# Kernel tuning notes

Measured on AMD Instinct MI355X. Metric: run time of the kernel, lower is better.

The kernel has to match this reference:

```python
import jax, jax.numpy as jnp
import numpy as np
import math

FS, N_FFT, NUM_BANDS, NUM_BINS = 16000, 512, 31, 257
H = 96  # dim_hidden

def band_partition():
    f_min, f_max = FS / N_FFT, FS / 2.0
    z_min = 69.0 + 12.0 * math.log2(f_min / 440.0)
    z_max = 69.0 + 12.0 * math.log2(f_max / 440.0)
    z = np.linspace(z_min, z_max, NUM_BANDS + 2)
    f_points = 440.0 * 2.0 ** ((z - 69.0) / 12.0)
    bins = np.round(f_points * N_FFT / FS).astype(np.int64)
    bins[0] = 0
    bands = []
    for i in range(NUM_BANDS):
        s = max(0, int(bins[i]))
        e = min(NUM_BINS, int(bins[i + 2]) + 1)
        if e <= s:
            e = s + 1
        bands.append((s, e))
    return bands

BANDS = band_partition()

def hann(L):
    # torch.hann_window default (periodic=True)
    return 0.5 - 0.5 * jnp.cos(2.0 * jnp.pi * jnp.arange(L, dtype=jnp.float32) / L)

def chan_ln(x, eps=1e-5):
    # AdaNorm2d assumed = LayerNorm over channel dim, no affine
    m = jnp.mean(x, axis=1, keepdims=True)
    v = jnp.var(x, axis=1, keepdims=True)
    return (x - m) * jax.lax.rsqrt(v + eps)

def prelu(x, a):
    return jnp.where(x >= 0, x, a * x)

def setup_inputs() -> dict:
    key = jax.random.key(0)
    ks = jax.random.split(key, 20)
    B, T = 4, 1000
    return {
        'mix_repr': jax.random.normal(ks[0], (B, H, NUM_BINS, T), jnp.float32),
        'spin': jax.random.normal(ks[1], (B, 64, NUM_BINS, T), jnp.float32),
        'doa': jax.random.normal(ks[2], (B, 36), jnp.float32),
        'enc_w': jax.random.normal(ks[3], (NUM_BANDS, H, 64), jnp.float32) * 0.05,
        'enc_b': jax.random.normal(ks[4], (NUM_BANDS, H), jnp.float32) * 0.05,
        'enc_a': 0.25 * jnp.ones((NUM_BANDS,), jnp.float32),
        'dqg_w': jax.random.normal(ks[5], (NUM_BANDS, 2 * H, 36), jnp.float32) * 0.05,
        'dqg_b': jax.random.normal(ks[6], (NUM_BANDS, 2 * H), jnp.float32) * 0.05,
        'dec_w': jax.random.normal(ks[7], (NUM_BANDS, H, H), jnp.float32) * 0.05,
        'dec_b': jax.random.normal(ks[8], (NUM_BANDS, H), jnp.float32) * 0.05,
        'dec_a': 0.25 * jnp.ones((NUM_BANDS,), jnp.float32),
        'qw': jax.random.normal(ks[9], (H, H), jnp.float32) * 0.05,
        'qb': jax.random.normal(ks[10], (H,), jnp.float32) * 0.05,
        'kw': jax.random.normal(ks[11], (H, H), jnp.float32) * 0.05,
        'kb': jax.random.normal(ks[12], (H,), jnp.float32) * 0.05,
        'vw': jax.random.normal(ks[13], (H, H), jnp.float32) * 0.05,
        'vb': jax.random.normal(ks[14], (H,), jnp.float32) * 0.05,
        'ow': jax.random.normal(ks[15], (H, H), jnp.float32) * 0.05,
        'ob': jax.random.normal(ks[16], (H,), jnp.float32) * 0.05,
    }

def reference(mix_repr, spin, doa, enc_w, enc_b, enc_a, dqg_w, dqg_b,
              dec_w, dec_b, dec_a, qw, qb, kw, kb, vw, vb, ow, ob):
    B, D, F, T = mix_repr.shape
    merged = jnp.zeros((B, H, F, T), mix_repr.dtype)
    wsum = jnp.zeros((F,), mix_repr.dtype)
    for k, (s, e) in enumerate(BANDS):  # fixed set of 31 static ragged bands
        L = e - s
        win = hann(L)
        sub = spin[:, :, s:e, :]                                   # [B,64,L,T]
        feat = jnp.einsum('oc,bcft->boft', enc_w[k], sub) + enc_b[k][None, :, None, None]
        feat = prelu(chan_ln(feat), enc_a[k])
        qp = doa @ dqg_w[k].T + dqg_b[k]                           # [B,2H]
        gamma, beta = qp[:, :H], qp[:, H:]
        tgt = (1.0 + gamma)[:, :, None, None] * feat + beta[:, :, None, None]
        dec = jnp.einsum('oc,bcft->boft', dec_w[k], tgt) + dec_b[k][None, :, None, None]
        dec = prelu(chan_ln(dec), dec_a[k])
        merged = merged.at[:, :, s:e, :].add(dec * win[None, None, :, None])
        wsum = wsum.at[s:e].add(win)
    merged = merged / jnp.clip(wsum, 1e-8)[None, None, :, None]
    # MixtureQueryFusion: 1x1 conv cross-attention gate
    Q = jnp.einsum('oc,bcft->boft', qw, mix_repr) + qb[None, :, None, None]
    K = jnp.einsum('oc,bcft->boft', kw, merged) + kb[None, :, None, None]
    V = jnp.einsum('oc,bcft->boft', vw, merged) + vb[None, :, None, None]
    attn = jax.nn.sigmoid(jnp.sum(Q * K, axis=1, keepdims=True) / jnp.sqrt(jnp.float32(H)))
    attended = V * attn
    out = mix_repr + jnp.einsum('oc,bcft->boft', ow, attended) + ob[None, :, None, None]
    return out
```

## Files before the change

### kernel.cpp

```cpp
#include <hip/hip_runtime.h>
#include <math.h>

#define NBANDS 31
#define FT 257000

typedef __attribute__((ext_vector_type(8))) short bh8;
typedef __attribute__((ext_vector_type(4))) float f4;

__constant__ int d_bs[NBANDS] = {0,1,1,2,2,2,3,3,4,5,6,7,8,10,11,13,16,19,23,27,32,38,45,54,64,76,91,108,128,152,181};
__constant__ int d_be[NBANDS] = {2,3,3,3,4,4,5,6,7,8,9,11,12,14,17,20,24,28,33,39,46,55,65,77,92,109,129,153,182,216,257};

__device__ __forceinline__ unsigned short b16u(float v) {
  __bf16 h = (__bf16)v;
  return __builtin_bit_cast(unsigned short, h);
}
__device__ __forceinline__ unsigned pk2(float a, float b) {
  return (unsigned)b16u(a) | ((unsigned)b16u(b) << 16);
}
__device__ __forceinline__ float hann1(int i, int L) {
  return 0.5f - 0.5f * cosf(6.283185307179586f * (float)i / (float)L);
}

__global__ __launch_bounds__(256) void prep_w(
    const float* __restrict__ enc_w, const float* __restrict__ dec_w,
    const float* __restrict__ qw, const float* __restrict__ kw,
    const float* __restrict__ vw, const float* __restrict__ ow,
    unsigned short* __restrict__ w16) {
  const int stride = gridDim.x * blockDim.x;
  for (int i = blockIdx.x * blockDim.x + threadIdx.x; i < 513024; i += stride) {
    float v;
    if (i < 190464) {
      const int k = i / 6144, r = i - k * 6144;
      const int tile = r >> 9, li = r & 511;
      const int lane = li >> 3, j = li & 7;
      const int g = lane >> 4, n = lane & 15;
      const int mt = tile >> 1, kt = tile & 1;
      v = enc_w[k * 6144 + (mt * 16 + n) * 64 + kt * 32 + g * 8 + j];
    } else if (i < 476160) {
      const int i2 = i - 190464;
      const int k = i2 / 9216, r = i2 - k * 9216;
      const int tile = r >> 9, li = r & 511;
      const int lane = li >> 3, j = li & 7;
      const int g = lane >> 4, n = lane & 15;
      const int mt = tile / 3, kt = tile - mt * 3;
      v = dec_w[k * 9216 + (mt * 16 + n) * 96 + kt * 32 + g * 8 + j];
    } else {
      const int i2 = i - 476160;
      const int a = i2 / 9216, r = i2 - a * 9216;
      const int tile = r >> 9, li = r & 511;
      const int lane = li >> 3, j = li & 7;
      const int g = lane >> 4, n = lane & 15;
      const int mt = tile / 3, kt = tile - mt * 3;
      const float* src = (a == 0) ? qw : (a == 1) ? kw : (a == 2) ? vw : ow;
      v = src[(mt * 16 + n) * 96 + kt * 32 + g * 8 + j];
    }
    w16[i] = b16u(v);
  }
}

__global__ __launch_bounds__(192) void qp_kernel(const float* __restrict__ doa,
                                                 const float* __restrict__ dqg_w,
                                                 const float* __restrict__ dqg_b,
                                                 float* __restrict__ gbuf) {
  const int k = blockIdx.x, b = blockIdx.y;
  const int tid = threadIdx.x;
  __shared__ float sdoa[36];
  if (tid < 36) sdoa[tid] = doa[b * 36 + tid];
  __syncthreads();
  const float* wr = dqg_w + (k * 192 + tid) * 36;
  float acc = dqg_b[k * 192 + tid];
  #pragma unroll
  for (int i = 0; i < 36; ++i) acc = fmaf(wr[i], sdoa[i], acc);
  if (tid < 96) acc += 1.0f;
  gbuf[(k * 4 + b) * 192 + tid] = acc;
}

__global__ __launch_bounds__(320) void tab_kernel(float* __restrict__ ftab) {
  const int f = blockIdx.x * blockDim.x + threadIdx.x;
  if (f >= 257) return;
  int k0 = 0; while (d_be[k0] <= f) ++k0;
  int k1 = k0; while (k1 < NBANDS && d_bs[k1] <= f) ++k1;
  float wsum = 0.f, wn[5];
  for (int k = k0; k < k1; ++k) {
    const float wv = hann1(f - d_bs[k], d_be[k] - d_bs[k]);
    wn[k - k0] = wv; wsum += wv;
  }
  float* o = ftab + f * 8;
  o[0] = (float)k0; o[1] = (float)(k1 - k0); o[2] = 1.0f / fmaxf(wsum, 1e-8f);
  #pragma unroll
  for (int j = 0; j < 5; ++j) o[3 + j] = (j < k1 - k0) ? wn[j] : 0.f;
}

#define LDSWAIT asm volatile("s_waitcnt lgkmcnt(0)" ::: "memory")

__device__ __forceinline__ void init6(f4* acc, const float* s, int off) {
  #pragma unroll
  for (int mt = 0; mt < 6; ++mt) {
    const float4 bb = *reinterpret_cast<const float4*>(s + mt * 16 + off);
    acc[mt] = (f4){bb.x, bb.y, bb.z, bb.w};
  }
}
__device__ __forceinline__ void ln96(const f4* acc, float& mean, float& rs) {
  float s0 = 0.f, s1 = 0.f, s2 = 0.f, s3 = 0.f;
  float q0 = 0.f, q1 = 0.f, q2 = 0.f, q3 = 0.f;
  #pragma unroll
  for (int mt = 0; mt < 6; ++mt) {
    const float a0 = acc[mt][0], a1 = acc[mt][1], a2 = acc[mt][2], a3 = acc[mt][3];
    s0 += a0; s1 += a1; s2 += a2; s3 += a3;
    q0 = fmaf(a0, a0, q0); q1 = fmaf(a1, a1, q1);
    q2 = fmaf(a2, a2, q2); q3 = fmaf(a3, a3, q3);
  }
  float sm = (s0 + s1) + (s2 + s3);
  float sq = (q0 + q1) + (q2 + q3);
  sm += __shfl_xor(sm, 16); sm += __shfl_xor(sm, 32);
  sq += __shfl_xor(sq, 16); sq += __shfl_xor(sq, 32);
  mean = sm * (1.f / 96.f);
  rs = rsqrtf(sq * (1.f / 96.f) - mean * mean + 1e-5f);
}
__device__ __forceinline__ void load6s(bh8* dst, const unsigned short* p, int step9) {
  #pragma unroll
  for (int mt = 0; mt < 6; ++mt)
    dst[mt] = *reinterpret_cast<const bh8*>(p + ((mt * step9) << 9));
}

__global__ __launch_bounds__(256, 3) void fused_mfma(
    const float* __restrict__ mix, const float* __restrict__ spin,
    const unsigned short* __restrict__ enc16, const float* __restrict__ enc_b, const float* __restrict__ enc_a,
    const unsigned short* __restrict__ dec16, const float* __restrict__ dec_b, const float* __restrict__ dec_a,
    const float* __restrict__ gb, const float* __restrict__ ftab,
    const unsigned short* __restrict__ q16, const float* __restrict__ qb,
    const unsigned short* __restrict__ k16, const float* __restrict__ kb,
    const unsigned short* __restrict__ v16, const float* __restrict__ vb,
    const unsigned short* __restrict__ o16, const float* __restrict__ ob,
    float* __restrict__ out) {
  const int id0 = (int)blockIdx.x;
  const int id  = (id0 & 7) * 2056 + (id0 >> 3);
  const int tt  = id & 15;
  const int fb  = id >> 4;
  const int f   = fb % 257;
  const int b   = fb / 257;
  const int t0  = tt << 6;

  const int tid  = threadIdx.x;
  const int lane = tid & 63;
  const int w    = tid >> 6;
  const int g    = lane >> 4;
  const int n    = lane & 15;
  const int col  = (w << 4) + n;
  const int t    = t0 + col;
  const bool tv  = t < 1000;
  const int tcl  = tv ? t : 999;
  const int sw   = (n & 7) << 3;
  const int lb   = lane << 3;

  __shared__ __align__(16) char smem[28160];
  unsigned short* XT = (unsigned short*)smem;
  float* stage = (float*)(smem + 16384);
  float* OS = (float*)smem;
  unsigned short* xw = XT + col * 128;

  const float* ft = ftab + f * 8;
  const int k0 = (int)ft[0];
  const int nb = (int)ft[1];
  const float winv = ft[2];

  {
    const int tot = (nb << 9) + 384;
    for (int i = tid; i < tot; i += 256) {
      const int kk = i >> 9, r = i & 511;
      float v = 0.f;
      if (kk < nb) {
        const int k = k0 + kk;
        if      (r < 96)  v = enc_b[k * 96 + r];
        else if (r < 192) v = dec_b[k * 96 + (r - 96)];
        else if (r < 384) v = gb[(k * 4 + b) * 192 + (r - 192)];
        else if (r == 384) v = enc_a[k];
        else if (r == 385) v = dec_a[k];
        else if (r == 386) v = ft[3 + kk];
      } else {
        const int r2 = i - (nb << 9);
        v = (r2 < 96) ? qb[r2] : (r2 < 192) ? kb[r2 - 96] : (r2 < 288) ? vb[r2 - 192] : ob[r2 - 288];
      }
      stage[i] = v;
    }
  }

  const float* spL = spin + b * 64 * FT + f * 1000 + tcl;
  const float* mxL = mix  + b * 96 * FT + f * 1000 + tcl;

  bh8 spb[2];
  {
    float spf[16];
    #pragma unroll
    for (int j = 0; j < 8; ++j) spf[j]     = __builtin_nontemporal_load(spL + (g * 8 + j) * FT);
    #pragma unroll
    for (int j = 0; j < 8; ++j) spf[8 + j] = __builtin_nontemporal_load(spL + (32 + g * 8 + j) * FT);
    #pragma unroll
    for (int kt = 0; kt < 2; ++kt)
      #pragma unroll
      for (int j = 0; j < 8; ++j) spb[kt][j] = (short)b16u(spf[kt * 8 + j]);
  }

  bh8 pre[6];
  load6s(pre, enc16 + k0 * 6144 + lb, 2);

  __syncthreads();

  f4 macc[6];
  #pragma unroll
  for (int mt = 0; mt < 6; ++mt) macc[mt] = (f4){0.f, 0.f, 0.f, 0.f};

  const int oo = g * 4;

  for (int kk = 0; kk < nb; ++kk) {
    const int k = k0 + kk;
    const unsigned short* ew  = enc16 + k * 6144 + lb;
    const unsigned short* dwp = dec16 + k * 9216 + lb;
    const float* stg = stage + (kk << 9);

    f4 acc[6];
    init6(acc, stg, oo);
    #pragma unroll
    for (int mt = 0; mt < 6; ++mt)
      acc[mt] = __builtin_amdgcn_mfma_f32_16x16x32_bf16(pre[mt], spb[0], acc[mt], 0, 0, 0);
    #pragma unroll
    for (int mt = 0; mt < 6; ++mt) {
      const bh8 af = *reinterpret_cast<const bh8*>(ew + ((mt * 2 + 1) << 9));
      acc[mt] = __builtin_amdgcn_mfma_f32_16x16x32_bf16(af, spb[1], acc[mt], 0, 0, 0);
    }

    load6s(pre, dwp, 3);

    float mean, rs;
    ln96(acc, mean, rs);
    const float ea = stg[384];
    #pragma unroll
    for (int mt = 0; mt < 6; ++mt) {
      const float4 ga = *reinterpret_cast<const float4*>(stg + 192 + mt * 16 + oo);
      const float4 be = *reinterpret_cast<const float4*>(stg + 288 + mt * 16 + oo);
      float x0 = (acc[mt][0] - mean) * rs; x0 = (x0 >= 0.f) ? x0 : ea * x0;
      float x1 = (acc[mt][1] - mean) * rs; x1 = (x1 >= 0.f) ? x1 : ea * x1;
      float x2 = (acc[mt][2] - mean) * rs; x2 = (x2 >= 0.f) ? x2 : ea * x2;
      float x3 = (acc[mt][3] - mean) * rs; x3 = (x3 >= 0.f) ? x3 : ea * x3;
      uint2 u;
      u.x = pk2(fmaf(ga.x, x0, be.x), fmaf(ga.y, x1, be.y));
      u.y = pk2(fmaf(ga.z, x2, be.z), fmaf(ga.w, x3, be.w));
      *reinterpret_cast<uint2*>(xw + ((mt * 16 + g * 4) ^ sw)) = u;
    }
    LDSWAIT;

    f4 dacc[6];
    init6(dacc, stg + 96, oo);
    {
      const bh8 bf0 = *reinterpret_cast<const bh8*>(xw + ((0 * 32 + g * 8) ^ sw));
      #pragma unroll
      for (int mt = 0; mt < 6; ++mt)
        dacc[mt] = __builtin_amdgcn_mfma_f32_16x16x32_bf16(pre[mt], bf0, dacc[mt], 0, 0, 0);
    }

    {
      const bool more = (kk + 1 < nb);
      load6s(pre, more ? (enc16 + (k + 1) * 6144 + lb) : (q16 + lb), more ? 2 : 3);
    }

    #pragma unroll
    for (int kt = 1; kt < 3; ++kt) {
      const bh8 bf = *reinterpret_cast<const bh8*>(xw + ((kt * 32 + g * 8) ^ sw));
      #pragma unroll
      for (int mt = 0; mt < 6; ++mt) {
        const bh8 af = *reinterpret_cast<const bh8*>(dwp + ((mt * 3 + kt) << 9));
        dacc[mt] = __builtin_amdgcn_mfma_f32_16x16x32_bf16(af, bf, dacc[mt], 0, 0, 0);
      }
    }
    float mean2, rs2;
    ln96(dacc, mean2, rs2);
    const float da = stg[385];
    const float win = stg[386];
    #pragma unroll
    for (int mt = 0; mt < 6; ++mt)
      #pragma unroll
      for (int r = 0; r < 4; ++r) {
        float x = (dacc[mt][r] - mean2) * rs2;
        x = (x >= 0.f) ? x : da * x;
        macc[mt][r] = fmaf(win, x, macc[mt][r]);
      }
  }

  float mxf[24];
  #pragma unroll
  for (int kt = 0; kt < 3; ++kt)
    #pragma unroll
    for (int j = 0; j < 8; ++j) mxf[kt * 8 + j] = mxL[(kt * 32 + g * 8 + j) * FT];

  #pragma unroll
  for (int mt = 0; mt < 6; ++mt) {
    uint2 u;
    u.x = pk2(macc[mt][0] * winv, macc[mt][1] * winv);
    u.y = pk2(macc[mt][2] * winv, macc[mt][3] * winv);
    *reinterpret_cast<uint2*>(xw + ((mt * 16 + g * 4) ^ sw)) = u;
  }
  LDSWAIT;
  bh8 gfr[3];
  #pragma unroll
  for (int kt = 0; kt < 3; ++kt) gfr[kt] = *reinterpret_cast<const bh8*>(xw + ((kt * 32 + g * 8) ^ sw));

  bh8 mxb[3];
  #pragma unroll
  for (int kt = 0; kt < 3; ++kt)
    #pragma unroll
    for (int j = 0; j < 8; ++j) mxb[kt][j] = (short)b16u(mxf[kt * 8 + j]);

  const float* stQ = stage + (nb << 9);

  f4 qacc[6];
  init6(qacc, stQ, oo);
  const unsigned short* qp16 = q16 + lb;
  #pragma unroll
  for (int mt = 0; mt < 6; ++mt)
    qacc[mt] = __builtin_amdgcn_mfma_f32_16x16x32_bf16(pre[mt], mxb[0], qacc[mt], 0, 0, 0);
  load6s(pre, k16 + lb, 3);
  #pragma unroll
  for (int kt = 1; kt < 3; ++kt)
    #pragma unroll
    for (int mt = 0; mt < 6; ++mt) {
      const bh8 af = *reinterpret_cast<const bh8*>(qp16 + ((mt * 3 + kt) << 9));
      qacc[mt] = __builtin_amdgcn_mfma_f32_16x16x32_bf16(af, mxb[kt], qacc[mt], 0, 0, 0);
    }
  f4 kacc[6];
  init6(kacc, stQ + 96, oo);
  const unsigned short* kp16 = k16 + lb;
  #pragma unroll
  for (int mt = 0; mt < 6; ++mt)
    kacc[mt] = __builtin_amdgcn_mfma_f32_16x16x32_bf16(pre[mt], gfr[0], kacc[mt], 0, 0, 0);
  load6s(pre, v16 + lb, 3);
  #pragma unroll
  for (int kt = 1; kt < 3; ++kt)
    #pragma unroll
    for (int mt = 0; mt < 6; ++mt) {
      const bh8 af = *reinterpret_cast<const bh8*>(kp16 + ((mt * 3 + kt) << 9));
      kacc[mt] = __builtin_amdgcn_mfma_f32_16x16x32_bf16(af, gfr[kt], kacc[mt], 0, 0, 0);
    }
  float p0 = 0.f, p1 = 0.f;
  #pragma unroll
  for (int mt = 0; mt < 6; ++mt) {
    p0 = fmaf(qacc[mt][0], kacc[mt][0], p0);
    p1 = fmaf(qacc[mt][1], kacc[mt][1], p1);
    p0 = fmaf(qacc[mt][2], kacc[mt][2], p0);
    p1 = fmaf(qacc[mt][3], kacc[mt][3], p1);
  }
  float p = p0 + p1;
  p += __shfl_xor(p, 16); p += __shfl_xor(p, 32);
  const float sig = 1.f / (1.f + __expf(-p * 0.10206207261596575f));

  f4 vacc[6];
  init6(vacc, stQ + 192, oo);
  const unsigned short* vp16 = v16 + lb;
  #pragma unroll
  for (int mt = 0; mt < 6; ++mt)
    vacc[mt] = __builtin_amdgcn_mfma_f32_16x16x32_bf16(pre[mt], gfr[0], vacc[mt], 0, 0, 0);
  load6s(pre, o16 + lb, 3);
  #pragma unroll
  for (int kt = 1; kt < 3; ++kt)
    #pragma unroll
    for (int mt = 0; mt < 6; ++mt) {
      const bh8 af = *reinterpret_cast<const bh8*>(vp16 + ((mt * 3 + kt) << 9));
      vacc[mt] = __builtin_amdgcn_mfma_f32_16x16x32_bf16(af, gfr[kt], vacc[mt], 0, 0, 0);
    }
  #pragma unroll
  for (int mt = 0; mt < 6; ++mt) {
    uint2 u;
    u.x = pk2(vacc[mt][0] * sig, vacc[mt][1] * sig);
    u.y = pk2(vacc[mt][2] * sig, vacc[mt][3] * sig);
    *reinterpret_cast<uint2*>(xw + ((mt * 16 + g * 4) ^ sw)) = u;
  }
  float mres[6][4];
  #pragma unroll
  for (int mt = 0; mt < 6; ++mt)
    #pragma unroll
    for (int r = 0; r < 4; ++r) mres[mt][r] = mxL[(mt * 16 + g * 4 + r) * FT];
  LDSWAIT;
  bh8 afr[3];
  #pragma unroll
  for (int kt = 0; kt < 3; ++kt) afr[kt] = *reinterpret_cast<const bh8*>(xw + ((kt * 32 + g * 8) ^ sw));

  f4 oacc[6];
  init6(oacc, stQ + 288, oo);
  const unsigned short* op16 = o16 + lb;
  #pragma unroll
  for (int mt = 0; mt < 6; ++mt)
    oacc[mt] = __builtin_amdgcn_mfma_f32_16x16x32_bf16(pre[mt], afr[0], oacc[mt], 0, 0, 0);
  #pragma unroll
  for (int kt = 1; kt < 3; ++kt)
    #pragma unroll
    for (int mt = 0; mt < 6; ++mt) {
      const bh8 af = *reinterpret_cast<const bh8*>(op16 + ((mt * 3 + kt) << 9));
      oacc[mt] = __builtin_amdgcn_mfma_f32_16x16x32_bf16(af, afr[kt], oacc[mt], 0, 0, 0);
    }

  __syncthreads();

  #pragma unroll
  for (int mt = 0; mt < 6; ++mt)
    #pragma unroll
    for (int r = 0; r < 4; ++r)
      OS[(mt * 16 + g * 4 + r) * 65 + col] = mres[mt][r] + oacc[mt][r];

  __syncthreads();

  const int cvalid = 1000 - t0;
  #pragma unroll
  for (int it = 0; it < 24; ++it) {
    const int i   = it * 256 + tid;
    const int row = i >> 6;
    const int c   = i & 63;
    const float val = OS[row * 65 + c];
    if (c < cvalid)
      __builtin_nontemporal_store(val, out + (b * 96 + row) * FT + f * 1000 + t0 + c);
  }
}

extern "C" void kernel_launch(void* const* d_in, const int* in_sizes, int n_in,
                              void* d_out, int out_size, void* d_ws, size_t ws_size,
                              hipStream_t stream) {
  (void)in_sizes; (void)n_in; (void)out_size; (void)ws_size;
  const float* mix   = (const float*)d_in[0];
  const float* spin  = (const float*)d_in[1];
  const float* doa   = (const float*)d_in[2];
  const float* enc_w = (const float*)d_in[3];
  const float* enc_b = (const float*)d_in[4];
  const float* enc_a = (const float*)d_in[5];
  const float* dqg_w = (const float*)d_in[6];
  const float* dqg_b = (const float*)d_in[7];
  const float* dec_w = (const float*)d_in[8];
  const float* dec_b = (const float*)d_in[9];
  const float* dec_a = (const float*)d_in[10];
  const float* qw    = (const float*)d_in[11];
  const float* qb    = (const float*)d_in[12];
  const float* kw    = (const float*)d_in[13];
  const float* kb    = (const float*)d_in[14];
  const float* vw    = (const float*)d_in[15];
  const float* vb    = (const float*)d_in[16];
  const float* oww   = (const float*)d_in[17];
  const float* obb   = (const float*)d_in[18];
  float* outp = (float*)d_out;

  unsigned short* w16 = (unsigned short*)d_ws;
  unsigned short* enc16 = w16;
  unsigned short* dec16 = w16 + 190464;
  unsigned short* q16   = w16 + 476160;
  unsigned short* k16   = q16 + 9216;
  unsigned short* v16   = k16 + 9216;
  unsigned short* o16   = v16 + 9216;
  float* gbws = (float*)((char*)d_ws + 1026048);
  float* ftab = (float*)((char*)d_ws + 1121280);

  hipLaunchKernelGGL(prep_w, dim3(512), dim3(256), 0, stream,
                     enc_w, dec_w, qw, kw, vw, oww, w16);
  hipLaunchKernelGGL(qp_kernel, dim3(NBANDS, 4), dim3(192), 0, stream,
                     doa, dqg_w, dqg_b, gbws);
  hipLaunchKernelGGL(tab_kernel, dim3(1), dim3(320), 0, stream, ftab);
  hipLaunchKernelGGL(fused_mfma, dim3(16448), dim3(256), 0, stream,
                     mix, spin, enc16, enc_b, enc_a, dec16, dec_b, dec_a, gbws, ftab,
                     q16, qb, k16, kb, v16, vb, o16, obb, outp);
}
```

Measured before the change: 541.1 us.

## Split output channels across two wave halves with 512-thread blocks

Doubles the block to 512 threads so each of two wave groups computes 48 of the 96 output channels per 16-column tile, halving per-thread accumulators and weight fragments. Channel LayerNorm and the Q·K dot product now combine partial sums through a small LDS buffer and extra __syncthreads barriers. The aim is lower register pressure and more waves in flight to hide memory latency, at the cost of several extra block-wide barriers inside the band loop and each thread loading the spin inputs redundantly.

```diff
diff --git a/kernel.cpp b/kernel.cpp
--- a/kernel.cpp
+++ b/kernel.cpp
@@ -91,39 +91,35 @@
   for (int j = 0; j < 5; ++j) o[3 + j] = (j < k1 - k0) ? wn[j] : 0.f;
 }
 
-#define LDSWAIT asm volatile("s_waitcnt lgkmcnt(0)" ::: "memory")
-
-__device__ __forceinline__ void init6(f4* acc, const float* s, int off) {
-  #pragma unroll
-  for (int mt = 0; mt < 6; ++mt) {
-    const float4 bb = *reinterpret_cast<const float4*>(s + mt * 16 + off);
-    acc[mt] = (f4){bb.x, bb.y, bb.z, bb.w};
-  }
-}
-__device__ __forceinline__ void ln96(const f4* acc, float& mean, float& rs) {
-  float s0 = 0.f, s1 = 0.f, s2 = 0.f, s3 = 0.f;
-  float q0 = 0.f, q1 = 0.f, q2 = 0.f, q3 = 0.f;
-  #pragma unroll
-  for (int mt = 0; mt < 6; ++mt) {
-    const float a0 = acc[mt][0], a1 = acc[mt][1], a2 = acc[mt][2], a3 = acc[mt][3];
-    s0 += a0; s1 += a1; s2 += a2; s3 += a3;
+__device__ __forceinline__ void load3s(bh8* dst, const unsigned short* p, int step9) {
+  #pragma unroll
+  for (int m = 0; m < 3; ++m)
+    dst[m] = *reinterpret_cast<const bh8*>(p + ((m * step9) << 9));
+}
+
+__device__ __forceinline__ void ln96x(const f4* acc, const int h, const int col,
+                                      const int g, float* red,
+                                      float& mean, float& rs) {
+  float s0 = 0.f, s1 = 0.f, q0 = 0.f, q1 = 0.f;
+  #pragma unroll
+  for (int m = 0; m < 3; ++m) {
+    const float a0 = acc[m][0], a1 = acc[m][1], a2 = acc[m][2], a3 = acc[m][3];
+    s0 += a0 + a2; s1 += a1 + a3;
     q0 = fmaf(a0, a0, q0); q1 = fmaf(a1, a1, q1);
-    q2 = fmaf(a2, a2, q2); q3 = fmaf(a3, a3, q3);
-  }
-  float sm = (s0 + s1) + (s2 + s3);
-  float sq = (q0 + q1) + (q2 + q3);
+    q0 = fmaf(a2, a2, q0); q1 = fmaf(a3, a3, q1);
+  }
+  float sm = s0 + s1, sq = q0 + q1;
   sm += __shfl_xor(sm, 16); sm += __shfl_xor(sm, 32);
   sq += __shfl_xor(sq, 16); sq += __shfl_xor(sq, 32);
+  if (g == 0) { red[h * 128 + col] = sm; red[h * 128 + 64 + col] = sq; }
+  __syncthreads();
+  sm += red[(1 - h) * 128 + col];
+  sq += red[(1 - h) * 128 + 64 + col];
   mean = sm * (1.f / 96.f);
   rs = rsqrtf(sq * (1.f / 96.f) - mean * mean + 1e-5f);
 }
-__device__ __forceinline__ void load6s(bh8* dst, const unsigned short* p, int step9) {
-  #pragma unroll
-  for (int mt = 0; mt < 6; ++mt)
-    dst[mt] = *reinterpret_cast<const bh8*>(p + ((mt * step9) << 9));
-}
-
-__global__ __launch_bounds__(256, 3) void fused_mfma(
+
+__global__ __launch_bounds__(512, 4) void fused_mfma(
     const float* __restrict__ mix, const float* __restrict__ spin,
     const unsigned short* __restrict__ enc16, const float* __restrict__ enc_b, const float* __restrict__ enc_a,
     const unsigned short* __restrict__ dec16, const float* __restrict__ dec_b, const float* __restrict__ dec_a,
@@ -143,20 +139,27 @@
 
   const int tid  = threadIdx.x;
   const int lane = tid & 63;
-  const int w    = tid >> 6;
+  const int wv   = tid >> 6;
+  const int cg   = wv & 3;
+  const int h    = wv >> 2;
   const int g    = lane >> 4;
   const int n    = lane & 15;
-  const int col  = (w << 4) + n;
+  const int col  = (cg << 4) + n;
   const int t    = t0 + col;
   const bool tv  = t < 1000;
   const int tcl  = tv ? t : 999;
   const int sw   = (n & 7) << 3;
   const int lb   = lane << 3;
-
-  __shared__ __align__(16) char smem[28160];
+  const int oo   = g * 4;
+  const int h48  = h * 48;
+  const int hb2  = (h * 6) << 9;
+  const int hb3  = (h * 9) << 9;
+
+  __shared__ __align__(16) char smem[30208];
   unsigned short* XT = (unsigned short*)smem;
   float* stage = (float*)(smem + 16384);
-  float* OS = (float*)smem;
+  float* red   = (float*)(smem + 28160);
+  float* OS    = (float*)smem;
   unsigned short* xw = XT + col * 128;
 
   const float* ft = ftab + f * 8;
@@ -166,7 +169,7 @@
 
   {
     const int tot = (nb << 9) + 384;
-    for (int i = tid; i < tot; i += 256) {
+    for (int i = tid; i < tot; i += 512) {
       const int kk = i >> 9, r = i & 511;
       float v = 0.f;
       if (kk < nb) {
@@ -201,88 +204,92 @@
       for (int j = 0; j < 8; ++j) spb[kt][j] = (short)b16u(spf[kt * 8 + j]);
   }
 
-  bh8 pre[6];
-  load6s(pre, enc16 + k0 * 6144 + lb, 2);
-
-  __syncthreads();
-
-  f4 macc[6];
-  #pragma unroll
-  for (int mt = 0; mt < 6; ++mt) macc[mt] = (f4){0.f, 0.f, 0.f, 0.f};
-
-  const int oo = g * 4;
+  bh8 pre[3];
+  load3s(pre, enc16 + k0 * 6144 + lb + hb2, 2);
+
+  __syncthreads();
+
+  f4 macc[3];
+  #pragma unroll
+  for (int m = 0; m < 3; ++m) macc[m] = (f4){0.f, 0.f, 0.f, 0.f};
 
   for (int kk = 0; kk < nb; ++kk) {
     const int k = k0 + kk;
-    const unsigned short* ew  = enc16 + k * 6144 + lb;
-    const unsigned short* dwp = dec16 + k * 9216 + lb;
+    const unsigned short* ewb = enc16 + k * 6144 + lb + hb2;
+    const unsigned short* dwb = dec16 + k * 9216 + lb + hb3;
     const float* stg = stage + (kk << 9);
 
-    f4 acc[6];
-    init6(acc, stg, oo);
-    #pragma unroll
-    for (int mt = 0; mt < 6; ++mt)
-      acc[mt] = __builtin_amdgcn_mfma_f32_16x16x32_bf16(pre[mt], spb[0], acc[mt], 0, 0, 0);
-    #pragma unroll
-    for (int mt = 0; mt < 6; ++mt) {
-      const bh8 af = *reinterpret_cast<const bh8*>(ew + ((mt * 2 + 1) << 9));
-      acc[mt] = __builtin_amdgcn_mfma_f32_16x16x32_bf16(af, spb[1], acc[mt], 0, 0, 0);
-    }
-
-    load6s(pre, dwp, 3);
+    f4 acc[3];
+    #pragma unroll
+    for (int m = 0; m < 3; ++m) {
+      const float4 bb = *reinterpret_cast<const float4*>(stg + h48 + m * 16 + oo);
+      acc[m] = (f4){bb.x, bb.y, bb.z, bb.w};
+    }
+    #pragma unroll
+    for (int m = 0; m < 3; ++m)
+      acc[m] = __builtin_amdgcn_mfma_f32_16x16x32_bf16(pre[m], spb[0], acc[m], 0, 0, 0);
+    #pragma unroll
+    for (int m = 0; m < 3; ++m) {
+      const bh8 af = *reinterpret_cast<const bh8*>(ewb + ((m * 2 + 1) << 9));
+      acc[m] = __builtin_amdgcn_mfma_f32_16x16x32_bf16(af, spb[1], acc[m], 0, 0, 0);
+    }
+
+    load3s(pre, dwb, 3);
 
     float mean, rs;
-    ln96(acc, mean, rs);
+    ln96x(acc, h, col, g, red, mean, rs);
     const float ea = stg[384];
     #pragma unroll
-    for (int mt = 0; mt < 6; ++mt) {
-      const float4 ga = *reinterpret_cast<const float4*>(stg + 192 + mt * 16 + oo);
-      const float4 be = *reinterpret_cast<const float4*>(stg + 288 + mt * 16 + oo);
-      float x0 = (acc[mt][0] - mean) * rs; x0 = (x0 >= 0.f) ? x0 : ea * x0;
-      float x1 = (acc[mt][1] - mean) * rs; x1 = (x1 >= 0.f) ? x1 : ea * x1;
-      float x2 = (acc[mt][2] - mean) * rs; x2 = (x2 >= 0.f) ? x2 : ea * x2;
-      float x3 = (acc[mt][3] - mean) * rs; x3 = (x3 >= 0.f) ? x3 : ea * x3;
+    for (int m = 0; m < 3; ++m) {
+      const float4 ga = *reinterpret_cast<const float4*>(stg + 192 + h48 + m * 16 + oo);
+      const float4 be = *reinterpret_cast<const float4*>(stg + 288 + h48 + m * 16 + oo);
+      float x0 = (acc[m][0] - mean) * rs; x0 = (x0 >= 0.f) ? x0 : ea * x0;
+      float x1 = (acc[m][1] - mean) * rs; x1 = (x1 >= 0.f) ? x1 : ea * x1;
+      float x2 = (acc[m][2] - mean) * rs; x2 = (x2 >= 0.f) ? x2 : ea * x2;
+      float x3 = (acc[m][3] - mean) * rs; x3 = (x3 >= 0.f) ? x3 : ea * x3;
       uint2 u;
       u.x = pk2(fmaf(ga.x, x0, be.x), fmaf(ga.y, x1, be.y));
       u.y = pk2(fmaf(ga.z, x2, be.z), fmaf(ga.w, x3, be.w));
-      *reinterpret_cast<uint2*>(xw + ((mt * 16 + g * 4) ^ sw)) = u;
-    }
-    LDSWAIT;
-
-    f4 dacc[6];
-    init6(dacc, stg + 96, oo);
+      *reinterpret_cast<uint2*>(xw + ((h48 + m * 16 + oo) ^ sw)) = u;
+    }
+    __syncthreads();
+
+    f4 dacc[3];
+    #pragma unroll
+    for (int m = 0; m < 3; ++m) {
+      const float4 bb = *reinterpret_cast<const float4*>(stg + 96 + h48 + m * 16 + oo);
+      dacc[m] = (f4){bb.x, bb.y, bb.z, bb.w};
+    }
     {
-      const bh8 bf0 = *reinterpret_cast<const bh8*>(xw + ((0 * 32 + g * 8) ^ sw));
+      const bh8 bf0 = *reinterpret_cast<const bh8*>(xw + ((g * 8) ^ sw));
       #pragma unroll
-      for (int mt = 0; mt < 6; ++mt)
-        dacc[mt] = __builtin_amdgcn_mfma_f32_16x16x32_bf16(pre[mt], bf0, dacc[mt], 0, 0, 0);
-    }
-
+      for (int m = 0; m < 3; ++m)
+        dacc[m] = __builtin_amdgcn_mfma_f32_16x16x32_bf16(pre[m], bf0, dacc[m], 0, 0, 0);
+    }
     {
       const bool more = (kk + 1 < nb);
-      load6s(pre, more ? (enc16 + (k + 1) * 6144 + lb) : (q16 + lb), more ? 2 : 3);
-    }
-
+      load3s(pre, more ? (enc16 + (k + 1) * 6144 + lb + hb2) : (q16 + lb + hb3), more ? 2 : 3);
+    }
     #pragma unroll
     for (int kt = 1; kt < 3; ++kt) {
       const bh8 bf = *reinterpret_cast<const bh8*>(xw + ((kt * 32 + g * 8) ^ sw));
       #pragma unroll
-      for (int mt = 0; mt < 6; ++mt) {
-        const bh8 af = *reinterpret_cast<const bh8*>(dwp + ((mt * 3 + kt) << 9));
-        dacc[mt] = __builtin_amdgcn_mfma_f32_16x16x32_bf16(af, bf, dacc[mt], 0, 0, 0);
+      for (int m = 0; m < 3; ++m) {
+        const bh8 af = *reinterpret_cast<const bh8*>(dwb + ((m * 3 + kt) << 9));
+        dacc[m] = __builtin_amdgcn_mfma_f32_16x16x32_bf16(af, bf, dacc[m], 0, 0, 0);
       }
     }
     float mean2, rs2;
-    ln96(dacc, mean2, rs2);
+    ln96x(dacc, h, col, g, red + 256, mean2, rs2);
     const float da = stg[385];
     const float win = stg[386];
     #pragma unroll
-    for (int mt = 0; mt < 6; ++mt)
+    for (int m = 0; m < 3; ++m)
       #pragma unroll
       for (int r = 0; r < 4; ++r) {
-        float x = (dacc[mt][r] - mean2) * rs2;
+        float x = (dacc[m][r] - mean2) * rs2;
         x = (x >= 0.f) ? x : da * x;
-        macc[mt][r] = fmaf(win, x, macc[mt][r]);
+        macc[m][r] = fmaf(win, x, macc[m][r]);
       }
   }
 
@@ -293,13 +300,13 @@
     for (int j = 0; j < 8; ++j) mxf[kt * 8 + j] = mxL[(kt * 32 + g * 8 + j) * FT];
 
   #pragma unroll
-  for (int mt = 0; mt < 6; ++mt) {
+  for (int m = 0; m < 3; ++m) {
     uint2 u;
-    u.x = pk2(macc[mt][0] * winv, macc[mt][1] * winv);
-    u.y = pk2(macc[mt][2] * winv, macc[mt][3] * winv);
-    *reinterpret_cast<uint2*>(xw + ((mt * 16 + g * 4) ^ sw)) = u;
-  }
-  LDSWAIT;
+    u.x = pk2(macc[m][0] * winv, macc[m][1] * winv);
+    u.y = pk2(macc[m][2] * winv, macc[m][3] * winv);
+    *reinterpret_cast<uint2*>(xw + ((h48 + m * 16 + oo) ^ sw)) = u;
+  }
+  __syncthreads();
   bh8 gfr[3];
   #pragma unroll
   for (int kt = 0; kt < 3; ++kt) gfr[kt] = *reinterpret_cast<const bh8*>(xw + ((kt * 32 + g * 8) ^ sw));
@@ -311,106 +318,125 @@
     for (int j = 0; j < 8; ++j) mxb[kt][j] = (short)b16u(mxf[kt * 8 + j]);
 
   const float* stQ = stage + (nb << 9);
-
-  f4 qacc[6];
-  init6(qacc, stQ, oo);
-  const unsigned short* qp16 = q16 + lb;
-  #pragma unroll
-  for (int mt = 0; mt < 6; ++mt)
-    qacc[mt] = __builtin_amdgcn_mfma_f32_16x16x32_bf16(pre[mt], mxb[0], qacc[mt], 0, 0, 0);
-  load6s(pre, k16 + lb, 3);
+  const unsigned short* qpb = q16 + lb + hb3;
+  const unsigned short* kpb = k16 + lb + hb3;
+  const unsigned short* vpb = v16 + lb + hb3;
+  const unsigned short* opb = o16 + lb + hb3;
+
+  f4 qacc[3];
+  #pragma unroll
+  for (int m = 0; m < 3; ++m) {
+    const float4 bb = *reinterpret_cast<const float4*>(stQ + h48 + m * 16 + oo);
+    qacc[m] = (f4){bb.x, bb.y, bb.z, bb.w};
+  }
+  #pragma unroll
+  for (int m = 0; m < 3; ++m)
+    qacc[m] = __builtin_amdgcn_mfma_f32_16x16x32_bf16(pre[m], mxb[0], qacc[m], 0, 0, 0);
+  load3s(pre, kpb, 3);
   #pragma unroll
   for (int kt = 1; kt < 3; ++kt)
     #pragma unroll
-    for (int mt = 0; mt < 6; ++mt) {
-      const bh8 af = *reinterpret_cast<const bh8*>(qp16 + ((mt * 3 + kt) << 9));
-      qacc[mt] = __builtin_amdgcn_mfma_f32_16x16x32_bf16(af, mxb[kt], qacc[mt], 0, 0, 0);
-    }
-  f4 kacc[6];
-  init6(kacc, stQ + 96, oo);
-  const unsigned short* kp16 = k16 + lb;
-  #pragma unroll
-  for (int mt = 0; mt < 6; ++mt)
-    kacc[mt] = __builtin_amdgcn_mfma_f32_16x16x32_bf16(pre[mt], gfr[0], kacc[mt], 0, 0, 0);
-  load6s(pre, v16 + lb, 3);
+    for (int m = 0; m < 3; ++m) {
+      const bh8 af = *reinterpret_cast<const bh8*>(qpb + ((m * 3 + kt) << 9));
+      qacc[m] = __builtin_amdgcn_mfma_f32_16x16x32_bf16(af, mxb[kt], qacc[m], 0, 0, 0);
+    }
+  f4 kacc[3];
+  #pragma unroll
+  for (int m = 0; m < 3; ++m) {
+    const float4 bb = *reinterpret_cast<const float4*>(stQ + 96 + h48 + m * 16 + oo);
+    kacc[m] = (f4){bb.x, bb.y, bb.z, bb.w};
+  }
+  #pragma unroll
+  for (int m = 0; m < 3; ++m)
+    kacc[m] = __builtin_amdgcn_mfma_f32_16x16x32_bf16(pre[m], gfr[0], kacc[m], 0, 0, 0);
+  load3s(pre, vpb, 3);
   #pragma unroll
   for (int kt = 1; kt < 3; ++kt)
     #pragma unroll
-    for (int mt = 0; mt < 6; ++mt) {
-      const bh8 af = *reinterpret_cast<const bh8*>(kp16 + ((mt * 3 + kt) << 9));
-      kacc[mt] = __builtin_amdgcn_mfma_f32_16x16x32_bf16(af, gfr[kt], kacc[mt], 0, 0, 0);
+    for (int m = 0; m < 3; ++m) {
+      const bh8 af = *reinterpret_cast<const bh8*>(kpb + ((m * 3 + kt) << 9));
+      kacc[m] = __builtin_amdgcn_mfma_f32_16x16x32_bf16(af, gfr[kt], kacc[m], 0, 0, 0);
     }
   float p0 = 0.f, p1 = 0.f;
   #pragma unroll
-  for (int mt = 0; mt < 6; ++mt) {
-    p0 = fmaf(qacc[mt][0], kacc[mt][0], p0);
-    p1 = fmaf(qacc[mt][1], kacc[mt][1], p1);
-    p0 = fmaf(qacc[mt][2], kacc[mt][2], p0);
-    p1 = fmaf(qacc[mt][3], kacc[mt][3], p1);
+  for (int m = 0; m < 3; ++m) {
+    p0 = fmaf(qacc[m][0], kacc[m][0], p0);
+    p1 = fmaf(qacc[m][1], kacc[m][1], p1);
+    p0 = fmaf(qacc[m][2], kacc[m][2], p0);
+    p1 = fmaf(qacc[m][3], kacc[m][3], p1);
   }
   float p = p0 + p1;
   p += __shfl_xor(p, 16); p += __shfl_xor(p, 32);
+  if (g == 0) red[h * 128 + col] = p;
+  __syncthreads();
+  p += red[(1 - h) * 128 + col];
   const float sig = 1.f / (1.f + __expf(-p * 0.10206207261596575f));
 
-  f4 vacc[6];
-  init6(vacc, stQ + 192, oo);
-  const unsigned short* vp16 = v16 + lb;
-  #pragma unroll
-  for (int mt = 0; mt < 6; ++mt)
-    vacc[mt] = __builtin_amdgcn_mfma_f32_16x16x32_bf16(pre[mt], gfr[0], vacc[mt], 0, 0, 0);
-  load6s(pre, o16 + lb, 3);
+  f4 vacc[3];
+  #pragma unroll
+  for (int m = 0; m < 3; ++m) {
+    const float4 bb = *reinterpret_cast<const float4*>(stQ + 192 + h48 + m * 16 + oo);
+    vacc[m] = (f4){bb.x, bb.y, bb.z, bb.w};
+  }
+  #pragma unroll
+  for (int m = 0; m < 3; ++m)
+    vacc[m] = __builtin_amdgcn_mfma_f32_16x16x32_bf16(pre[m], gfr[0], vacc[m], 0, 0, 0);
+  load3s(pre, opb, 3);
   #pragma unroll
   for (int kt = 1; kt < 3; ++kt)
     #pragma unroll
-    for (int mt = 0; mt < 6; ++mt) {
-      const bh8 af = *reinterpret_cast<const bh8*>(vp16 + ((mt * 3 + kt) << 9));
-      vacc[mt] = __builtin_amdgcn_mfma_f32_16x16x32_bf16(af, gfr[kt], vacc[mt], 0, 0, 0);
-    }
-  #pragma unroll
-  for (int mt = 0; mt < 6; ++mt) {
+    for (int m = 0; m < 3; ++m) {
+      const bh8 af = *reinterpret_cast<const bh8*>(vpb + ((m * 3 + kt) << 9));
+      vacc[m] = __builtin_amdgcn_mfma_f32_16x16x32_bf16(af, gfr[kt], vacc[m], 0, 0, 0);
+    }
+  #pragma unroll
+  for (int m = 0; m < 3; ++m) {
     uint2 u;
-    u.x = pk2(vacc[mt][0] * sig, vacc[mt][1] * sig);
-    u.y = pk2(vacc[mt][2] * sig, vacc[mt][3] * sig);
-    *reinterpret_cast<uint2*>(xw + ((mt * 16 + g * 4) ^ sw)) = u;
-  }
-  float mres[6][4];
-  #pragma unroll
-  for (int mt = 0; mt < 6; ++mt)
-    #pragma unroll
-    for (int r = 0; r < 4; ++r) mres[mt][r] = mxL[(mt * 16 + g * 4 + r) * FT];
-  LDSWAIT;
+    u.x = pk2(vacc[m][0] * sig, vacc[m][1] * sig);
+    u.y = pk2(vacc[m][2] * sig, vacc[m][3] * sig);
+    *reinterpret_cast<uint2*>(xw + ((h48 + m * 16 + oo) ^ sw)) = u;
+  }
+  float mres[3][4];
+  #pragma unroll
+  for (int m = 0; m < 3; ++m)
+    #pragma unroll
+    for (int r = 0; r < 4; ++r) mres[m][r] = mxL[(h48 + m * 16 + oo + r) * FT];
+  __syncthreads();
   bh8 afr[3];
   #pragma unroll
   for (int kt = 0; kt < 3; ++kt) afr[kt] = *reinterpret_cast<const bh8*>(xw + ((kt * 32 + g * 8) ^ sw));
 
-  f4 oacc[6];
-  init6(oacc, stQ + 288, oo);
-  const unsigned short* op16 = o16 + lb;
-  #pragma unroll
-  for (int mt = 0; mt < 6; ++mt)
-    oacc[mt] = __builtin_amdgcn_mfma_f32_16x16x32_bf16(pre[mt], afr[0], oacc[mt], 0, 0, 0);
+  f4 oacc[3];
+  #pragma unroll
+  for (int m = 0; m < 3; ++m) {
+    const float4 bb = *reinterpret_cast<const float4*>(stQ + 288 + h48 + m * 16 + oo);
+    oacc[m] = (f4){bb.x, bb.y, bb.z, bb.w};
+  }
+  #pragma unroll
+  for (int m = 0; m < 3; ++m)
+    oacc[m] = __builtin_amdgcn_mfma_f32_16x16x32_bf16(pre[m], afr[0], oacc[m], 0, 0, 0);
   #pragma unroll
   for (int kt = 1; kt < 3; ++kt)
     #pragma unroll
-    for (int mt = 0; mt < 6; ++mt) {
-      const bh8 af = *reinterpret_cast<const bh8*>(op16 + ((mt * 3 + kt) << 9));
-      oacc[mt] = __builtin_amdgcn_mfma_f32_16x16x32_bf16(af, afr[kt], oacc[mt], 0, 0, 0);
-    }
-
-  __syncthreads();
-
-  #pragma unroll
-  for (int mt = 0; mt < 6; ++mt)
+    for (int m = 0; m < 3; ++m) {
+      const bh8 af = *reinterpret_cast<const bh8*>(opb + ((m * 3 + kt) << 9));
+      oacc[m] = __builtin_amdgcn_mfma_f32_16x16x32_bf16(af, afr[kt], oacc[m], 0, 0, 0);
+    }
+
+  __syncthreads();
+
+  #pragma unroll
+  for (int m = 0; m < 3; ++m)
     #pragma unroll
     for (int r = 0; r < 4; ++r)
-      OS[(mt * 16 + g * 4 + r) * 65 + col] = mres[mt][r] + oacc[mt][r];
+      OS[(h48 + m * 16 + oo + r) * 65 + col] = mres[m][r] + oacc[m][r];
 
   __syncthreads();
 
   const int cvalid = 1000 - t0;
   #pragma unroll
-  for (int it = 0; it < 24; ++it) {
-    const int i   = it * 256 + tid;
+  for (int it = 0; it < 12; ++it) {
+    const int i   = it * 512 + tid;
     const int row = i >> 6;
     const int c   = i & 63;
     const float val = OS[row * 65 + c];
@@ -459,7 +485,7 @@
   hipLaunchKernelGGL(qp_kernel, dim3(NBANDS, 4), dim3(192), 0, stream,
                      doa, dqg_w, dqg_b, gbws);
   hipLaunchKernelGGL(tab_kernel, dim3(1), dim3(320), 0, stream, ftab);
-  hipLaunchKernelGGL(fused_mfma, dim3(16448), dim3(256), 0, stream,
+  hipLaunchKernelGGL(fused_mfma, dim3(16448), dim3(512), 0, stream,
                      mix, spin, enc16, enc_b, enc_a, dec16, dec_b, dec_a, gbws, ftab,
                      q16, qb, k16, kb, v16, vb, o16, obb, outp);
 }
```

Measured after the change: 613.4 us. 13.4% more time.
